# Kernel optimization log

Measured on AMD Instinct MI355X. Metric: run time of the kernel, lower is better.

Reference implementation:

```python
import jax, jax.numpy as jnp
import numpy as np

SIZE = 784          # number of MPS sites (pixels)
D = 32              # bond dimension
EMB_D = 2           # local feature dim, embedding x -> [1-x, x]
NUM_LABELS = 10
LABEL_SITE = SIZE // 2
BATCH = 128
INIT_STD = 0.01     # matches default 'random_eye' init


def setup_inputs() -> dict:
    key = jax.random.key(0)
    k1, k2, k3 = jax.random.split(key, 3)
    # raw pixel values in [0,1] so the affine embedding is valid
    batch_input = jax.random.uniform(k1, (BATCH, SIZE), dtype=jnp.float32)
    eye = jnp.eye(D, dtype=jnp.float32)
    # 'random_eye' init: identity (broadcast over site & physical dims) + small noise.
    # Keeps the 784-long matrix chain numerically well-conditioned.
    core_tensors = eye[None, :, None, :] + INIT_STD * jax.random.normal(
        k2, (SIZE, D, EMB_D, D), dtype=jnp.float32)
    label_tensor = eye[:, None, :] + INIT_STD * jax.random.normal(
        k3, (D, NUM_LABELS, D), dtype=jnp.float32)
    return {"batch_input": batch_input,
            "core_tensors": core_tensors,
            "label_tensor": label_tensor}


def _chain_matmul(mats):
    """Ordered product M_0 @ M_1 @ ... @ M_{n-1} via log-depth pairwise tree.
    mats: [B, n, D, D] -> [B, D, D]. n is static, so the Python while is fine."""
    while mats.shape[1] > 1:
        n = mats.shape[1]
        half = n // 2
        prod = jnp.matmul(mats[:, 0:2 * half:2], mats[:, 1:2 * half:2])
        if n % 2:
            prod = jnp.concatenate([prod, mats[:, -1:]], axis=1)
        mats = prod
    return mats[:, 0]


def reference(batch_input, core_tensors, label_tensor):
    # embedding_map: x -> [1-x, x]                                  [B, S, d]
    emb = jnp.stack([1.0 - batch_input, batch_input], axis=-1)
    # _contract_batch_input: per-site matrices M[b,s] = sum_d core[s,:,d,:]*emb[b,s,d]
    mats = jnp.einsum('sadc,bsd->bsac', core_tensors, emb)       # [B, S, D, D]
    left = _chain_matmul(mats[:, :LABEL_SITE])                    # [B, D, D]
    right = _chain_matmul(mats[:, LABEL_SITE:])                   # [B, D, D]
    # periodic bc: out[b,l] = trace(left @ T_l @ right)
    return jnp.einsum('bij,jlk,bki->bl', left, label_tensor, right)  # [B, num_labels]
```

## Files before the change

kernel.cpp:

```cpp
#include <hip/hip_runtime.h>
#include <stdint.h>

typedef float f32x16 __attribute__((ext_vector_type(16)));
typedef short bf16x8 __attribute__((ext_vector_type(8)));
typedef uint32_t u32;
typedef uint32_t u32x4 __attribute__((ext_vector_type(4)));

#define SIZE 784
#define NLBL 10
#define LABEL_SITE 392
#define BATCH 128
#define PRE_ELEMS (SIZE * 2 * 64 * 4)
#define LSTR 33
#define LSLOT (LSTR * 32)

#if defined(__has_builtin)
#if __has_builtin(__builtin_amdgcn_permlane32_swap)
#define HAVE_PLSWAP 1
#endif
#endif
#ifndef HAVE_PLSWAP
#define HAVE_PLSWAP 0
#endif


__device__ inline u32 cvt_pk(float a, float b) {
  u32 r;
  asm("v_cvt_pk_bf16_f32 %0, %1, %2" : "=v"(r) : "v"(a), "v"(b));
  return r;
}
__device__ inline float lo16f(u32 h) { return __uint_as_float(h << 16); }
__device__ inline float hi16f(u32 h) { return __uint_as_float(h & 0xffff0000u); }

__device__ inline void split_pack(const float s[8], u32 hi[4], u32 lo[4]) {
#pragma unroll
  for (int p = 0; p < 4; ++p) {
    u32 h = cvt_pk(s[2 * p], s[2 * p + 1]);
    hi[p] = h;
    lo[p] = cvt_pk(s[2 * p] - lo16f(h), s[2 * p + 1] - hi16f(h));
  }
}

__device__ inline f32x16 mfma_bb(const u32 (&a)[4], const u32 (&b)[4], f32x16 c) {
  union U { u32 u[4]; bf16x8 v; };
  U A, B;
#pragma unroll
  for (int i = 0; i < 4; ++i) { A.u[i] = a[i]; B.u[i] = b[i]; }
  return __builtin_amdgcn_mfma_f32_32x32x16_bf16(A.v, B.v, c, 0, 0, 0);
}
__device__ inline f32x16 mfma_v4(u32x4 a, const u32 (&b)[4], f32x16 c) {
  union UA { u32x4 u; bf16x8 v; } A; A.u = a;
  union UB { u32 u[4]; bf16x8 v; } B;
#pragma unroll
  for (int i = 0; i < 4; ++i) B.u[i] = b[i];
  return __builtin_amdgcn_mfma_f32_32x32x16_bf16(A.v, B.v, c, 0, 0, 0);
}

__device__ inline f32x16 ident_acc(int lane) {
  const int gam = lane & 31, hib = lane >> 5;
  f32x16 a;
#pragma unroll
  for (int reg = 0; reg < 16; ++reg) {
    int rho = (reg & 3) + 8 * (reg >> 2) + 4 * hib;
    a[reg] = (rho == gam) ? 1.0f : 0.0f;
  }
  return a;
}

__device__ inline int probe_mode(int lane) {
#if HAVE_PLSWAP
  u32 a = (u32)lane, b = (u32)(64 + lane);
  auto r = __builtin_amdgcn_permlane32_swap(a, b, false, false);
  u32 eLo = (u32)(lane + (lane & 32));
  u32 eHi = (u32)(lane + 32 + (lane & 32));
  if (__all(r[0] == eLo) && __all(r[1] == eHi)) return 1;
  if (__all(r[0] == eHi) && __all(r[1] == eLo)) return 2;
#endif
  return 0;
}

template <int MODE>
__device__ inline void build_b(const f32x16& acc, int hib, int t,
                               u32 (&Bh)[4], u32 (&Bl)[4]) {
  float slot[8];
#pragma unroll
  for (int j = 0; j < 4; ++j) {
    const int q1 = 8 * t + j, q2 = q1 + 4;
#if HAVE_PLSWAP
    if (MODE != 0) {
      u32 au = __float_as_uint(acc[q1]), bu = __float_as_uint(acc[q2]);
      auto r = __builtin_amdgcn_permlane32_swap(au, bu, false, false);
      slot[j]     = __uint_as_float(MODE == 1 ? r[0] : r[1]);
      slot[j + 4] = __uint_as_float(MODE == 1 ? r[1] : r[0]);
    } else
#endif
    {
      float z = hib ? acc[q1] : acc[q2];
      float wv = __shfl_xor(z, 32, 64);
      slot[j]     = hib ? wv : acc[q1];
      slot[j + 4] = hib ? acc[q2] : wv;
    }
  }
  split_pack(slot, Bh, Bl);
}

template <int MODE>
__device__ inline f32x16 chain_step(const u32 (&Ah)[2][4], const u32 (&Al)[2][4],
                                    f32x16 acc, int hib) {
  f32x16 r;
#pragma unroll
  for (int q = 0; q < 16; ++q) r[q] = 0.0f;
#pragma unroll
  for (int t = 0; t < 2; ++t) {
    u32 Bh[4], Bl[4];
    build_b<MODE>(acc, hib, t, Bh, Bl);
    r = mfma_bb(Al[t], Bh, r);
    r = mfma_bb(Ah[t], Bl, r);
    r = mfma_bb(Ah[t], Bh, r);
  }
  return r;
}

__device__ inline void store_cd(float* dst, f32x16 acc, int lane) {
  const int gam = lane & 31, hib = lane >> 5;
#pragma unroll
  for (int reg = 0; reg < 16; ++reg) {
    int rho = (reg & 3) + 8 * (reg >> 2) + 4 * hib;
    dst[rho * 32 + gam] = acc[reg];
  }
}

__device__ inline void store_cd33(float* dst, f32x16 acc, int lane) {
  const int gam = lane & 31, hib = lane >> 5;
#pragma unroll
  for (int reg = 0; reg < 16; ++reg) {
    int rho = (reg & 3) + 8 * (reg >> 2) + 4 * hib;
    dst[rho * LSTR + gam] = acc[reg];
  }
}
__device__ inline f32x16 load_cd33(const float* src, int lane) {
  const int gam = lane & 31, hib = lane >> 5;
  f32x16 a;
#pragma unroll
  for (int reg = 0; reg < 16; ++reg) {
    int rho = (reg & 3) + 8 * (reg >> 2) + 4 * hib;
    a[reg] = src[rho * LSTR + gam];
  }
  return a;
}
__device__ inline void load_afrag_lds33(const float* src, int lane,
                                        u32 (&Ah)[2][4], u32 (&Al)[2][4]) {
  const int row = lane & 31, hb8 = (lane >> 5) * 8;
#pragma unroll
  for (int h = 0; h < 2; ++h) {
    float v[8];
#pragma unroll
    for (int j = 0; j < 8; ++j) v[j] = src[row * LSTR + h * 16 + hb8 + j];
    split_pack(v, Ah[h], Al[h]);
  }
}

__device__ inline void load_afrag_rm(const float* src, int lane,
                                     u32 (&Ah)[2][4], u32 (&Al)[2][4]) {
  const int row = lane & 31, hb8 = (lane >> 5) * 8;
#pragma unroll
  for (int h = 0; h < 2; ++h) {
    const float* p = src + row * 32 + h * 16 + hb8;
    float4 q0 = *(const float4*)p;
    float4 q1 = *(const float4*)(p + 4);
    float v[8] = {q0.x, q0.y, q0.z, q0.w, q1.x, q1.y, q1.z, q1.w};
    split_pack(v, Ah[h], Al[h]);
  }
}

__global__ __launch_bounds__(256) void mps_precomp(const float* __restrict__ core,
                                                   u32* __restrict__ pc0h,
                                                   u32* __restrict__ pc0l,
                                                   u32* __restrict__ pdh,
                                                   u32* __restrict__ pdl) {
  const int tid = threadIdx.x;
  const int w = tid >> 6, lane = tid & 63;
  const int task = blockIdx.x * 4 + w;
  const int s = task >> 1, t = task & 1;
  const int r = lane & 31, hib = lane >> 5;
  const float* cs = core + (size_t)s * 2048 + r;
  u32 wc0h[4], wc0l[4], wdh[4], wdl[4];
#pragma unroll
  for (int p = 0; p < 4; ++p) {
    const int k0 = 16 * t + 8 * hib + 2 * p;
    float a0 = cs[k0 * 64],       a1 = cs[(k0 + 1) * 64];
    float b0 = cs[k0 * 64 + 32],  b1 = cs[(k0 + 1) * 64 + 32];
    float d0 = b0 - a0, d1 = b1 - a1;
    u32 h = cvt_pk(a0, a1);
    wc0h[p] = h;
    wc0l[p] = cvt_pk(a0 - lo16f(h), a1 - hi16f(h));
    u32 gg = cvt_pk(d0, d1);
    wdh[p] = gg;
    wdl[p] = cvt_pk(d0 - lo16f(gg), d1 - hi16f(gg));
  }
  const size_t base = ((size_t)task * 64 + lane) * 4;
  *(u32x4*)(pc0h + base) = *(u32x4*)wc0h;
  *(u32x4*)(pc0l + base) = *(u32x4*)wc0l;
  *(u32x4*)(pdh  + base) = *(u32x4*)wdh;
  *(u32x4*)(pdl  + base) = *(u32x4*)wdl;
}

struct Frags {
  u32x4 C0h[2], C0l[2], Dh[2], Dl[2];
  float x;
};

__device__ inline void load_frags(Frags& F,
                                  const u32* __restrict__ pc0h, const u32* __restrict__ pc0l,
                                  const u32* __restrict__ pdh,  const u32* __restrict__ pdl,
                                  const float* __restrict__ input, int bi, int s, int lane) {
  F.x = input[(size_t)bi * SIZE + s];
#pragma unroll
  for (int t = 0; t < 2; ++t) {
    const size_t base = ((size_t)(s * 2 + t) * 64 + lane) * 4;
    F.C0h[t] = *(const u32x4*)(pc0h + base);
    F.C0l[t] = *(const u32x4*)(pc0l + base);
    F.Dh[t]  = *(const u32x4*)(pdh + base);
    F.Dl[t]  = *(const u32x4*)(pdl + base);
  }
}

template <int MODE>
__device__ inline void do_step(f32x16& acc, const Frags& F, int hib) {
  f32x16 rc, rd;
#pragma unroll
  for (int q = 0; q < 16; ++q) { rc[q] = 0.0f; rd[q] = 0.0f; }
#pragma unroll
  for (int t = 0; t < 2; ++t) {
    u32 Bh[4], Bl[4];
    build_b<MODE>(acc, hib, t, Bh, Bl);
    rd = mfma_v4(F.Dl[t], Bh, rd);
    rd = mfma_v4(F.Dh[t], Bl, rd);
    rd = mfma_v4(F.Dh[t], Bh, rd);
    rc = mfma_v4(F.C0l[t], Bh, rc);
    rc = mfma_v4(F.C0h[t], Bl, rc);
    rc = mfma_v4(F.C0h[t], Bh, rc);
  }
#pragma unroll
  for (int q = 0; q < 16; ++q) acc[q] = fmaf(F.x, rd[q], rc[q]);
}

template <int SEGLEN, int MODE>
__device__ void phase1_body(const float* __restrict__ input,
                            const u32* __restrict__ pc0h, const u32* __restrict__ pc0l,
                            const u32* __restrict__ pdh,  const u32* __restrict__ pdl,
                            float* __restrict__ wsA, int nseg,
                            int lane, int bi, int g) {
  const int hib = lane >> 5;
  f32x16 acc = ident_acc(lane);
  const int ci0 = g * SEGLEN;
  int s0 = LABEL_SITE + ci0;
  if (s0 >= SIZE) s0 -= SIZE;
  Frags FA, FB;
  load_frags(FA, pc0h, pc0l, pdh, pdl, input, bi, s0, lane);
#pragma unroll
  for (int i = 0; i < SEGLEN; ++i) {
    int sn = LABEL_SITE + ci0 + i + 1;
    if (sn >= SIZE) sn -= SIZE;
    if ((i & 1) == 0) {
      if (i + 1 < SEGLEN) load_frags(FB, pc0h, pc0l, pdh, pdl, input, bi, sn, lane);
      do_step<MODE>(acc, FA, hib);
    } else {
      if (i + 1 < SEGLEN) load_frags(FA, pc0h, pc0l, pdh, pdl, input, bi, sn, lane);
      do_step<MODE>(acc, FB, hib);
    }
  }
  store_cd(wsA + ((size_t)bi * nseg + g) * 1024, acc, lane);
}

template <int SEGLEN>
__global__ __launch_bounds__(256) void mps_phase1(
    const float* __restrict__ input,
    const u32* __restrict__ pc0h, const u32* __restrict__ pc0l,
    const u32* __restrict__ pdh,  const u32* __restrict__ pdl,
    float* __restrict__ wsA, int nseg) {
  const int tid = threadIdx.x;
  const int w = tid >> 6, lane = tid & 63;
  const int g = blockIdx.x % nseg, c = blockIdx.x / nseg;
  const int bi = c * 4 + w;
  const int mode = probe_mode(lane);
  if (mode == 1)
    phase1_body<SEGLEN, 1>(input, pc0h, pc0l, pdh, pdl, wsA, nseg, lane, bi, g);
  else if (mode == 2)
    phase1_body<SEGLEN, 2>(input, pc0h, pc0l, pdh, pdl, wsA, nseg, lane, bi, g);
  else
    phase1_body<SEGLEN, 0>(input, pc0h, pc0l, pdh, pdl, wsA, nseg, lane, bi, g);
}

template <int MODE>
__device__ void phase2_body(const float* __restrict__ wsA,
                            const float* __restrict__ label,
                            float* __restrict__ out, int nseg,
                            int lane, int w, int bi, float* lds) {
  const int per = nseg / 8;
  f32x16 acc = ident_acc(lane);
  for (int g = w * per; g < (w + 1) * per; ++g) {
    u32 Ah[2][4], Al[2][4];
    load_afrag_rm(wsA + ((size_t)bi * nseg + g) * 1024, lane, Ah, Al);
    acc = chain_step<MODE>(Ah, Al, acc, lane >> 5);
  }
  store_cd33(lds + w * LSLOT, acc, lane);
  __syncthreads();
  f32x16 na;
#pragma unroll
  for (int lvl = 4; lvl >= 1; lvl >>= 1) {
    const bool act = (w < lvl);
    if (act) {
      f32x16 a = load_cd33(lds + (2 * w) * LSLOT, lane);
      u32 Ah[2][4], Al[2][4];
      load_afrag_lds33(lds + (2 * w + 1) * LSLOT, lane, Ah, Al);
      na = chain_step<MODE>(Ah, Al, a, lane >> 5);
    }
    __syncthreads();
    if (act) store_cd33(lds + w * LSLOT, na, lane);
    __syncthreads();
  }
  if (w == 0) {
    const int gam = lane & 31, hib = lane >> 5;
    float part[NLBL];
#pragma unroll
    for (int l = 0; l < NLBL; ++l) part[l] = 0.0f;
#pragma unroll
    for (int reg = 0; reg < 16; ++reg) {
      const int rho = (reg & 3) + 8 * (reg >> 2) + 4 * hib;
      const float wv = na[reg];
      const float* tp = label + rho * (NLBL * 32) + gam;
#pragma unroll
      for (int l = 0; l < NLBL; ++l) part[l] = fmaf(tp[l * 32], wv, part[l]);
    }
#pragma unroll
    for (int l = 0; l < NLBL; ++l) {
#pragma unroll
      for (int mask = 32; mask >= 1; mask >>= 1)
        part[l] += __shfl_xor(part[l], mask, 64);
    }
    if (lane == 0) {
#pragma unroll
      for (int l = 0; l < NLBL; ++l) out[bi * NLBL + l] = part[l];
    }
  }
}

__global__ __launch_bounds__(512) void mps_phase2(const float* __restrict__ wsA,
                                                  const float* __restrict__ label,
                                                  float* __restrict__ out, int nseg) {
  __shared__ float lds[8 * LSLOT];
  const int tid = threadIdx.x;
  const int w = tid >> 6, lane = tid & 63;
  const int bi = blockIdx.x;
  const int mode = probe_mode(lane);
  if (mode == 1)      phase2_body<1>(wsA, label, out, nseg, lane, w, bi, lds);
  else if (mode == 2) phase2_body<2>(wsA, label, out, nseg, lane, w, bi, lds);
  else                phase2_body<0>(wsA, label, out, nseg, lane, w, bi, lds);
}

extern "C" void kernel_launch(void* const* d_in, const int* in_sizes, int n_in,
                              void* d_out, int out_size, void* d_ws, size_t ws_size,
                              hipStream_t stream) {
  const float* input = (const float*)d_in[0];
  const float* core  = (const float*)d_in[1];
  const float* label = (const float*)d_in[2];
  float* out = (float*)d_out;

  u32* pc0h = (u32*)d_ws;
  u32* pc0l = pc0h + PRE_ELEMS;
  u32* pdh  = pc0l + PRE_ELEMS;
  u32* pdl  = pdh + PRE_ELEMS;
  float* wsA = (float*)(pdl + PRE_ELEMS);

  const size_t need112 = ((size_t)4 * PRE_ELEMS + (size_t)BATCH * 112 * 1024) * 4;
  const int nseg = (ws_size >= need112) ? 112 : 56;

  mps_precomp<<<dim3(392), dim3(256), 0, stream>>>(core, pc0h, pc0l, pdh, pdl);
  if (nseg == 112)
    mps_phase1<7><<<dim3(112 * 32), dim3(256), 0, stream>>>(input, pc0h, pc0l, pdh, pdl,
                                                            wsA, 112);
  else
    mps_phase1<14><<<dim3(56 * 32), dim3(256), 0, stream>>>(input, pc0h, pc0l, pdh, pdl,
                                                            wsA, 56);
  mps_phase2<<<dim3(BATCH), dim3(512), 0, stream>>>(wsA, label, out, nseg);
}
```

Baseline: 72.30 us.

## Split phase-2 reduction into wide group pass and seed segments from first site

Each segment's accumulator now starts from the first site's matrix, built directly as c0 + x*(c1-c0) from precomputed fp32 tables. This removes one identity-times-matrix MFMA step per segment. The serial phase-2 chain, where 8 waves per batch each walked nseg/8 segment products, is split in two. A new mps_phase2a kernel runs BATCH*ngroups waves, each reducing GG segments with prefetched loads, and a smaller final kernel combines the group products and applies the label contraction. This adds an extra launch and workspace round trip in exchange for more parallelism across the GPU.

```diff
diff --git a/kernel.cpp b/kernel.cpp
--- a/kernel.cpp
+++ b/kernel.cpp
@@ -11,6 +11,7 @@
 #define LABEL_SITE 392
 #define BATCH 128
 #define PRE_ELEMS (SIZE * 2 * 64 * 4)
+#define MAXSEG 112
 #define LSTR 33
 #define LSLOT (LSTR * 32)
 
@@ -24,6 +25,12 @@
 #endif
 
 
+__device__ inline int site_of(int ci) {
+  int s = LABEL_SITE + ci;
+  if (s >= SIZE) s -= SIZE;
+  return s;
+}
+
 __device__ inline u32 cvt_pk(float a, float b) {
   u32 r;
   asm("v_cvt_pk_bf16_f32 %0, %1, %2" : "=v"(r) : "v"(a), "v"(b));
@@ -54,17 +61,6 @@
 #pragma unroll
   for (int i = 0; i < 4; ++i) B.u[i] = b[i];
   return __builtin_amdgcn_mfma_f32_32x32x16_bf16(A.v, B.v, c, 0, 0, 0);
-}
-
-__device__ inline f32x16 ident_acc(int lane) {
-  const int gam = lane & 31, hib = lane >> 5;
-  f32x16 a;
-#pragma unroll
-  for (int reg = 0; reg < 16; ++reg) {
-    int rho = (reg & 3) + 8 * (reg >> 2) + 4 * hib;
-    a[reg] = (rho == gam) ? 1.0f : 0.0f;
-  }
-  return a;
 }
 
 __device__ inline int probe_mode(int lane) {
@@ -130,6 +126,42 @@
   }
 }
 
+__device__ inline f32x16 load_cd_rm(const float* src, int lane) {
+  const int gam = lane & 31, hib = lane >> 5;
+  f32x16 a;
+#pragma unroll
+  for (int reg = 0; reg < 16; ++reg) {
+    int rho = (reg & 3) + 8 * (reg >> 2) + 4 * hib;
+    a[reg] = src[rho * 32 + gam];
+  }
+  return a;
+}
+
+__device__ inline void load_raw(float4 (&q)[4], const float* src, int lane) {
+  const int row = lane & 31, hb8 = (lane >> 5) * 8;
+  const float* p = src + row * 32 + hb8;
+  q[0] = *(const float4*)(p);
+  q[1] = *(const float4*)(p + 4);
+  q[2] = *(const float4*)(p + 16);
+  q[3] = *(const float4*)(p + 20);
+}
+__device__ inline void split_raw(const float4 (&q)[4],
+                                 u32 (&Ah)[2][4], u32 (&Al)[2][4]) {
+#pragma unroll
+  for (int h = 0; h < 2; ++h) {
+    float v[8] = {q[2 * h].x, q[2 * h].y, q[2 * h].z, q[2 * h].w,
+                  q[2 * h + 1].x, q[2 * h + 1].y, q[2 * h + 1].z, q[2 * h + 1].w};
+    split_pack(v, Ah[h], Al[h]);
+  }
+}
+
+__device__ inline void load_afrag_rm(const float* src, int lane,
+                                     u32 (&Ah)[2][4], u32 (&Al)[2][4]) {
+  float4 q[4];
+  load_raw(q, src, lane);
+  split_raw(q, Ah, Al);
+}
+
 __device__ inline void store_cd33(float* dst, f32x16 acc, int lane) {
   const int gam = lane & 31, hib = lane >> 5;
 #pragma unroll
@@ -156,19 +188,6 @@
     float v[8];
 #pragma unroll
     for (int j = 0; j < 8; ++j) v[j] = src[row * LSTR + h * 16 + hb8 + j];
-    split_pack(v, Ah[h], Al[h]);
-  }
-}
-
-__device__ inline void load_afrag_rm(const float* src, int lane,
-                                     u32 (&Ah)[2][4], u32 (&Al)[2][4]) {
-  const int row = lane & 31, hb8 = (lane >> 5) * 8;
-#pragma unroll
-  for (int h = 0; h < 2; ++h) {
-    const float* p = src + row * 32 + h * 16 + hb8;
-    float4 q0 = *(const float4*)p;
-    float4 q1 = *(const float4*)(p + 4);
-    float v[8] = {q0.x, q0.y, q0.z, q0.w, q1.x, q1.y, q1.z, q1.w};
     split_pack(v, Ah[h], Al[h]);
   }
 }
@@ -177,7 +196,10 @@
                                                    u32* __restrict__ pc0h,
                                                    u32* __restrict__ pc0l,
                                                    u32* __restrict__ pdh,
-                                                   u32* __restrict__ pdl) {
+                                                   u32* __restrict__ pdl,
+                                                   float* __restrict__ pcd0,
+                                                   float* __restrict__ pcdd,
+                                                   int seglen) {
   const int tid = threadIdx.x;
   const int w = tid >> 6, lane = tid & 63;
   const int task = blockIdx.x * 4 + w;
@@ -203,6 +225,21 @@
   *(u32x4*)(pc0l + base) = *(u32x4*)wc0l;
   *(u32x4*)(pdh  + base) = *(u32x4*)wdh;
   *(u32x4*)(pdl  + base) = *(u32x4*)wdl;
+
+  const int ci = (s + LABEL_SITE) % SIZE;
+  if (ci % seglen == 0) {
+    const int g = ci / seglen;
+    const int gam = lane & 31;
+#pragma unroll
+    for (int rr = 0; rr < 8; ++rr) {
+      const int reg = 8 * t + rr;
+      const int rho = (reg & 3) + 8 * (reg >> 2) + 4 * hib;
+      float c0v = core[(size_t)s * 2048 + gam * 64 + rho];
+      float c1v = core[(size_t)s * 2048 + gam * 64 + 32 + rho];
+      pcd0[g * 1024 + rho * 32 + gam] = c0v;
+      pcdd[g * 1024 + rho * 32 + gam] = c1v - c0v;
+    }
+  }
 }
 
 struct Frags {
@@ -249,24 +286,34 @@
 __device__ void phase1_body(const float* __restrict__ input,
                             const u32* __restrict__ pc0h, const u32* __restrict__ pc0l,
                             const u32* __restrict__ pdh,  const u32* __restrict__ pdl,
+                            const float* __restrict__ pcd0, const float* __restrict__ pcdd,
                             float* __restrict__ wsA, int nseg,
                             int lane, int bi, int g) {
   const int hib = lane >> 5;
-  f32x16 acc = ident_acc(lane);
+  const int gam = lane & 31;
   const int ci0 = g * SEGLEN;
-  int s0 = LABEL_SITE + ci0;
-  if (s0 >= SIZE) s0 -= SIZE;
   Frags FA, FB;
-  load_frags(FA, pc0h, pc0l, pdh, pdl, input, bi, s0, lane);
-#pragma unroll
-  for (int i = 0; i < SEGLEN; ++i) {
-    int sn = LABEL_SITE + ci0 + i + 1;
-    if (sn >= SIZE) sn -= SIZE;
-    if ((i & 1) == 0) {
-      if (i + 1 < SEGLEN) load_frags(FB, pc0h, pc0l, pdh, pdl, input, bi, sn, lane);
+  load_frags(FA, pc0h, pc0l, pdh, pdl, input, bi, site_of(ci0 + 1), lane);
+  const float x0 = input[(size_t)bi * SIZE + site_of(ci0)];
+  f32x16 acc;
+  {
+    const float* p0 = pcd0 + g * 1024;
+    const float* pd = pcdd + g * 1024;
+#pragma unroll
+    for (int reg = 0; reg < 16; ++reg) {
+      const int rho = (reg & 3) + 8 * (reg >> 2) + 4 * hib;
+      acc[reg] = fmaf(x0, pd[rho * 32 + gam], p0[rho * 32 + gam]);
+    }
+  }
+#pragma unroll
+  for (int i = 1; i < SEGLEN; ++i) {
+    if (((i - 1) & 1) == 0) {
+      if (i + 1 < SEGLEN)
+        load_frags(FB, pc0h, pc0l, pdh, pdl, input, bi, site_of(ci0 + i + 1), lane);
       do_step<MODE>(acc, FA, hib);
     } else {
-      if (i + 1 < SEGLEN) load_frags(FA, pc0h, pc0l, pdh, pdl, input, bi, sn, lane);
+      if (i + 1 < SEGLEN)
+        load_frags(FA, pc0h, pc0l, pdh, pdl, input, bi, site_of(ci0 + i + 1), lane);
       do_step<MODE>(acc, FB, hib);
     }
   }
@@ -278,6 +325,7 @@
     const float* __restrict__ input,
     const u32* __restrict__ pc0h, const u32* __restrict__ pc0l,
     const u32* __restrict__ pdh,  const u32* __restrict__ pdl,
+    const float* __restrict__ pcd0, const float* __restrict__ pcdd,
     float* __restrict__ wsA, int nseg) {
   const int tid = threadIdx.x;
   const int w = tid >> 6, lane = tid & 63;
@@ -285,24 +333,62 @@
   const int bi = c * 4 + w;
   const int mode = probe_mode(lane);
   if (mode == 1)
-    phase1_body<SEGLEN, 1>(input, pc0h, pc0l, pdh, pdl, wsA, nseg, lane, bi, g);
+    phase1_body<SEGLEN, 1>(input, pc0h, pc0l, pdh, pdl, pcd0, pcdd, wsA, nseg, lane, bi, g);
   else if (mode == 2)
-    phase1_body<SEGLEN, 2>(input, pc0h, pc0l, pdh, pdl, wsA, nseg, lane, bi, g);
+    phase1_body<SEGLEN, 2>(input, pc0h, pc0l, pdh, pdl, pcd0, pcdd, wsA, nseg, lane, bi, g);
   else
-    phase1_body<SEGLEN, 0>(input, pc0h, pc0l, pdh, pdl, wsA, nseg, lane, bi, g);
+    phase1_body<SEGLEN, 0>(input, pc0h, pc0l, pdh, pdl, pcd0, pcdd, wsA, nseg, lane, bi, g);
 }
 
 template <int MODE>
-__device__ void phase2_body(const float* __restrict__ wsA,
-                            const float* __restrict__ label,
-                            float* __restrict__ out, int nseg,
-                            int lane, int w, int bi, float* lds) {
-  const int per = nseg / 8;
-  f32x16 acc = ident_acc(lane);
-  for (int g = w * per; g < (w + 1) * per; ++g) {
+__device__ void phase2a_body(const float* __restrict__ wsA, float* __restrict__ wsB,
+                             int nseg, int GG, int ngroups,
+                             int lane, int bi, int gg) {
+  const float* srcb = wsA + ((size_t)bi * nseg + gg * GG) * 1024;
+  f32x16 acc = load_cd_rm(srcb, lane);
+  float4 qa[4];
+  load_raw(qa, srcb + 1024, lane);
+  for (int k = 1; k < GG; ++k) {
+    float4 qb[4];
+    if (k + 1 < GG) load_raw(qb, srcb + (size_t)(k + 1) * 1024, lane);
     u32 Ah[2][4], Al[2][4];
-    load_afrag_rm(wsA + ((size_t)bi * nseg + g) * 1024, lane, Ah, Al);
+    split_raw(qa, Ah, Al);
     acc = chain_step<MODE>(Ah, Al, acc, lane >> 5);
+    if (k + 1 < GG) { qa[0] = qb[0]; qa[1] = qb[1]; qa[2] = qb[2]; qa[3] = qb[3]; }
+  }
+  store_cd(wsB + ((size_t)bi * ngroups + gg) * 1024, acc, lane);
+}
+
+__global__ __launch_bounds__(256) void mps_phase2a(const float* __restrict__ wsA,
+                                                   float* __restrict__ wsB,
+                                                   int nseg, int GG, int ngroups) {
+  const int tid = threadIdx.x;
+  const int w = tid >> 6, lane = tid & 63;
+  const int wid = blockIdx.x * 4 + w;
+  const int bi = wid & 127, gg = wid >> 7;
+  const int mode = probe_mode(lane);
+  if (mode == 1)      phase2a_body<1>(wsA, wsB, nseg, GG, ngroups, lane, bi, gg);
+  else if (mode == 2) phase2a_body<2>(wsA, wsB, nseg, GG, ngroups, lane, bi, gg);
+  else                phase2a_body<0>(wsA, wsB, nseg, GG, ngroups, lane, bi, gg);
+}
+
+template <int MODE>
+__device__ void phase2f_body(const float* __restrict__ wsB,
+                             const float* __restrict__ label,
+                             float* __restrict__ out, int ngroups,
+                             int lane, int w, int bi, float* lds) {
+  f32x16 acc;
+  if (ngroups == 14) {
+    if (w < 6) {
+      acc = load_cd_rm(wsB + ((size_t)bi * 14 + 2 * w) * 1024, lane);
+      u32 Ah[2][4], Al[2][4];
+      load_afrag_rm(wsB + ((size_t)bi * 14 + 2 * w + 1) * 1024, lane, Ah, Al);
+      acc = chain_step<MODE>(Ah, Al, acc, lane >> 5);
+    } else {
+      acc = load_cd_rm(wsB + ((size_t)bi * 14 + 6 + w) * 1024, lane);
+    }
+  } else {
+    acc = load_cd_rm(wsB + ((size_t)bi * ngroups + w) * 1024, lane);
   }
   store_cd33(lds + w * LSLOT, acc, lane);
   __syncthreads();
@@ -346,17 +432,18 @@
   }
 }
 
-__global__ __launch_bounds__(512) void mps_phase2(const float* __restrict__ wsA,
-                                                  const float* __restrict__ label,
-                                                  float* __restrict__ out, int nseg) {
+__global__ __launch_bounds__(512) void mps_phase2f(const float* __restrict__ wsB,
+                                                   const float* __restrict__ label,
+                                                   float* __restrict__ out,
+                                                   int ngroups) {
   __shared__ float lds[8 * LSLOT];
   const int tid = threadIdx.x;
   const int w = tid >> 6, lane = tid & 63;
   const int bi = blockIdx.x;
   const int mode = probe_mode(lane);
-  if (mode == 1)      phase2_body<1>(wsA, label, out, nseg, lane, w, bi, lds);
-  else if (mode == 2) phase2_body<2>(wsA, label, out, nseg, lane, w, bi, lds);
-  else                phase2_body<0>(wsA, label, out, nseg, lane, w, bi, lds);
+  if (mode == 1)      phase2f_body<1>(wsB, label, out, ngroups, lane, w, bi, lds);
+  else if (mode == 2) phase2f_body<2>(wsB, label, out, ngroups, lane, w, bi, lds);
+  else                phase2f_body<0>(wsB, label, out, ngroups, lane, w, bi, lds);
 }
 
 extern "C" void kernel_launch(void* const* d_in, const int* in_sizes, int n_in,
@@ -371,17 +458,27 @@
   u32* pc0l = pc0h + PRE_ELEMS;
   u32* pdh  = pc0l + PRE_ELEMS;
   u32* pdl  = pdh + PRE_ELEMS;
-  float* wsA = (float*)(pdl + PRE_ELEMS);
-
-  const size_t need112 = ((size_t)4 * PRE_ELEMS + (size_t)BATCH * 112 * 1024) * 4;
-  const int nseg = (ws_size >= need112) ? 112 : 56;
-
-  mps_precomp<<<dim3(392), dim3(256), 0, stream>>>(core, pc0h, pc0l, pdh, pdl);
-  if (nseg == 112)
-    mps_phase1<7><<<dim3(112 * 32), dim3(256), 0, stream>>>(input, pc0h, pc0l, pdh, pdl,
-                                                            wsA, 112);
+  float* pcd0 = (float*)(pdl + PRE_ELEMS);
+  float* pcdd = pcd0 + (size_t)MAXSEG * 1024;
+  float* wsA  = pcdd + (size_t)MAXSEG * 1024;
+
+  const size_t base_elems = (size_t)4 * PRE_ELEMS + (size_t)2 * MAXSEG * 1024;
+  const size_t need112 = (base_elems + (size_t)BATCH * 112 * 1024 +
+                          (size_t)BATCH * 14 * 1024) * 4;
+  int nseg, seglen, GG, ngroups;
+  if (ws_size >= need112) { nseg = 112; seglen = 7;  GG = 8; ngroups = 14; }
+  else                    { nseg = 56;  seglen = 14; GG = 7; ngroups = 8;  }
+  float* wsB = wsA + (size_t)BATCH * nseg * 1024;
+
+  mps_precomp<<<dim3(392), dim3(256), 0, stream>>>(core, pc0h, pc0l, pdh, pdl,
+                                                   pcd0, pcdd, seglen);
+  if (seglen == 7)
+    mps_phase1<7><<<dim3(nseg * 32), dim3(256), 0, stream>>>(
+        input, pc0h, pc0l, pdh, pdl, pcd0, pcdd, wsA, nseg);
   else
-    mps_phase1<14><<<dim3(56 * 32), dim3(256), 0, stream>>>(input, pc0h, pc0l, pdh, pdl,
-                                                            wsA, 56);
-  mps_phase2<<<dim3(BATCH), dim3(512), 0, stream>>>(wsA, label, out, nseg);
-}
+    mps_phase1<14><<<dim3(nseg * 32), dim3(256), 0, stream>>>(
+        input, pc0h, pc0l, pdh, pdl, pcd0, pcdd, wsA, nseg);
+  mps_phase2a<<<dim3((BATCH * ngroups) / 4), dim3(256), 0, stream>>>(
+      wsA, wsB, nseg, GG, ngroups);
+  mps_phase2f<<<dim3(BATCH), dim3(512), 0, stream>>>(wsB, label, out, ngroups);
+}
```

After: 70.09 us. -3.1%, faster.
